# Kernel tuning notes

Measured on AMD Instinct MI355X. Metric: run time of the kernel, lower is better.

## Reference

```python
import jax, jax.numpy as jnp
import numpy as np

B, S, D, H, HD = 2, 1024, 1024, 16, 64
CKV, CQ, R, DFF, L, V = 256, 384, 32, 2816, 4, 32000
EPS = 1.1920929e-07  # torch RMSNorm default eps = finfo(float32).eps


def rmsnorm(x, w):
    return x * jax.lax.rsqrt(jnp.mean(x * x, -1, keepdims=True) + EPS) * w


def rope(x, base=10000.0):
    # x: [B, H, S, d]; GPT-NeoX style rotate-half, matches RoPE._neg_half
    d, s = x.shape[-1], x.shape[2]
    theta = 1.0 / base ** (jnp.arange(0, d, 2, dtype=jnp.float32) / d)
    ang = jnp.arange(s, dtype=jnp.float32)[:, None] * theta[None, :]
    ang = jnp.concatenate([ang, ang], -1)  # [s, d]
    neg = jnp.concatenate([-x[..., d // 2:], x[..., :d // 2]], -1)
    return x * jnp.cos(ang) + neg * jnp.sin(ang)


def forward(tokens, embed, w_kv_down, b_kv_down, w_q_down, b_q_down, w_kv_up, b_kv_up,
            w_q_up, b_q_up, w_o, b_o, kv_norm_w, q_norm_w, norm1_w, norm2_w,
            w_in, b_in, w_out, b_out, norm_f_w, w_head, b_head):
    h = embed[tokens]                                  # [B, S, D]
    causal = jnp.triu(jnp.ones((S, S), bool), 1)       # True above diagonal -> masked
    scale = np.float32(1.0 / np.sqrt(HD + R))
    for i in range(L):
        xn = rmsnorm(h, norm1_w[i])
        ckv = xn @ w_kv_down[i] + b_kv_down[i]         # [B, S, CKV+R]
        c_kv, k_rope = ckv[..., :CKV], ckv[..., CKV:]
        kv = rmsnorm(c_kv, kv_norm_w[i]) @ w_kv_up[i] + b_kv_up[i]
        kv = kv.reshape(B, S, H, 2 * HD).transpose(0, 2, 1, 3)  # [B, H, S, 2*HD]
        k, v = kv[..., :HD], kv[..., HD:]
        qf = rmsnorm(xn @ w_q_down[i] + b_q_down[i], q_norm_w[i]) @ w_q_up[i] + b_q_up[i]
        qf = qf.reshape(B, S, H, HD + R).transpose(0, 2, 1, 3)   # [B, H, S, HD+R]
        q, q_rope = qf[..., :HD], qf[..., HD:]
        k_rope = rope(k_rope[:, None, :, :])           # [B, 1, S, R], shared across heads
        q_rope = rope(q_rope)
        k = jnp.concatenate([k, jnp.broadcast_to(k_rope, (B, H, S, R))], -1)
        q = jnp.concatenate([q, q_rope], -1)
        a = jnp.einsum('bhqd,bhkd->bhqk', q, k) * scale
        a = jax.nn.softmax(jnp.where(causal, -jnp.inf, a), -1)
        attn = jnp.einsum('bhqk,bhkd->bhqd', a, v).transpose(0, 2, 1, 3).reshape(B, S, D)
        h = h + attn @ w_o[i] + b_o[i]
        uv = rmsnorm(h, norm2_w[i]) @ w_in[i] + b_in[i]  # [B, S, 2*DFF]
        h = h + (uv[..., :DFF] * jax.nn.silu(uv[..., DFF:])) @ w_out[i] + b_out[i]
    return rmsnorm(h, norm_f_w) @ w_head + b_head        # [B, S, V]


def setup_inputs() -> dict:
    key = jax.random.key(0)
    it = iter(jax.random.split(key, 24))
    w = lambda shp: jax.random.normal(next(it), shp, jnp.float32) * 0.02
    return dict(
        tokens=jax.random.randint(next(it), (B, S), 0, V),
        embed=w((V, D)),
        w_kv_down=w((L, D, CKV + R)), b_kv_down=w((L, CKV + R)),
        w_q_down=w((L, D, CQ)), b_q_down=w((L, CQ)),
        w_kv_up=w((L, CKV, 2 * HD * H)), b_kv_up=w((L, 2 * HD * H)),
        w_q_up=w((L, CQ, (HD + R) * H)), b_q_up=w((L, (HD + R) * H)),
        w_o=w((L, D, D)), b_o=w((L, D)),
        kv_norm_w=jnp.ones((L, CKV)), q_norm_w=jnp.ones((L, CQ)),
        norm1_w=jnp.ones((L, D)), norm2_w=jnp.ones((L, D)),
        w_in=w((L, D, 2 * DFF)), b_in=w((L, 2 * DFF)),
        w_out=w((L, DFF, D)), b_out=w((L, D)),
        norm_f_w=jnp.ones((D,)),
        w_head=w((D, V)), b_head=w((V,)),
    )


def reference(tokens, embed, w_kv_down, b_kv_down, w_q_down, b_q_down, w_kv_up, b_kv_up,
              w_q_up, b_q_up, w_o, b_o, kv_norm_w, q_norm_w, norm1_w, norm2_w,
              w_in, b_in, w_out, b_out, norm_f_w, w_head, b_head):
    return forward(tokens, embed, w_kv_down, b_kv_down, w_q_down, b_q_down, w_kv_up,
                   b_kv_up, w_q_up, b_q_up, w_o, b_o, kv_norm_w, q_norm_w, norm1_w,
                   norm2_w, w_in, b_in, w_out, b_out, norm_f_w, w_head, b_head)
```

## Files before the change

### kernel.cpp

```cpp
#include <hip/hip_runtime.h>
#include <cstdint>
#include <cstddef>

typedef unsigned short u16;
typedef __attribute__((__ext_vector_type__(8))) __bf16 bf16x8;
typedef __attribute__((__ext_vector_type__(4))) float f32x4;
typedef __attribute__((__ext_vector_type__(8))) unsigned short u16x8;

#define DEVI __device__ __forceinline__

constexpr int Bb = 2, Ss = 1024, Dd = 1024, Hh = 16;
constexpr int Mm = Bb * Ss;
constexpr int QKD = 128;
constexpr float EPSF = 1.1920929e-07f;
constexpr float NEG = -1e30f;
constexpr float QSCALE = 0.10206207261596577f;
constexpr float LOG1E4_16 = 9.210340371976184f / 16.f;

DEVI u16 f2b(float f) {
  union { float f; uint32_t u; } a; a.f = f;
  uint32_t r = a.u + 0x7FFFu + ((a.u >> 16) & 1u);
  return (u16)(r >> 16);
}
DEVI float b2f(u16 h) {
  union { uint32_t u; float f; } a; a.u = ((uint32_t)h) << 16; return a.f;
}

struct WJob { const float* src; u16* dst; int K; int N; int perm; int ntiles; };
struct WJobs { WJob j[7]; };

__global__ __launch_bounds__(256) void k_wcvt_batch(WJobs jobs, int njobs) {
  int t = blockIdx.x;
  int ji = 0;
  while (ji < njobs - 1 && t >= jobs.j[ji].ntiles) { t -= jobs.j[ji].ntiles; ++ji; }
  const float* __restrict__ src = jobs.j[ji].src;
  u16* __restrict__ dst = jobs.j[ji].dst;
  const int K = jobs.j[ji].K, N = jobs.j[ji].N, perm = jobs.j[ji].perm;
  const int ktiles = K >> 6;
  const int bk = (t % ktiles) * 64;
  const int bn = (t / ktiles) * 64;
  __shared__ float ts[64][65];
  const int tid = threadIdx.x;
  {
    int c4 = tid & 15, r = tid >> 4;
    #pragma unroll
    for (int p = 0; p < 4; ++p) {
      int row = r + p * 16;
      int col = bn + c4 * 4;
      float4 v = make_float4(0.f, 0.f, 0.f, 0.f);
      if (col < N) v = *(const float4*)(src + (size_t)(bk + row) * N + col);
      ts[row][c4 * 4 + 0] = v.x; ts[row][c4 * 4 + 1] = v.y;
      ts[row][c4 * 4 + 2] = v.z; ts[row][c4 * 4 + 3] = v.w;
    }
  }
  __syncthreads();
  {
    int k8 = tid & 7, c = tid >> 3;
    #pragma unroll
    for (int p = 0; p < 2; ++p) {
      int cc = c + p * 32;
      int gcol = bn + cc;
      int row = perm ? ((gcol < 2816) ? (gcol * 2) : ((gcol - 2816) * 2 + 1)) : gcol;
      u16x8 o;
      #pragma unroll
      for (int q = 0; q < 8; ++q) o[q] = f2b(ts[k8 * 8 + q][cc]);
      *(u16x8*)(dst + (size_t)row * K + bk + k8 * 8) = o;
    }
  }
}

__global__ void k_embed(const int* __restrict__ tok, const float* __restrict__ emb,
                        float* __restrict__ h) {
  int m = blockIdx.x;
  int t = tok[m];
  const float4* src = (const float4*)(emb + (size_t)t * Dd);
  float4* dst = (float4*)(h + (size_t)m * Dd);
  dst[threadIdx.x] = src[threadIdx.x];
}

__global__ void k_rms(const float* __restrict__ in, int inStride,
                      const float* __restrict__ w, u16* __restrict__ out, int K) {
  int m = blockIdx.x;
  const float* x = in + (size_t)m * inStride;
  float ss = 0.f;
  for (int i = threadIdx.x; i < K; i += 256) { float v = x[i]; ss += v * v; }
  #pragma unroll
  for (int off = 32; off; off >>= 1) ss += __shfl_xor(ss, off);
  __shared__ float red[4];
  if ((threadIdx.x & 63) == 0) red[threadIdx.x >> 6] = ss;
  __syncthreads();
  float r = rsqrtf((red[0] + red[1] + red[2] + red[3]) / (float)K + EPSF);
  for (int i = threadIdx.x; i < K; i += 256)
    out[(size_t)m * K + i] = f2b(x[i] * r * w[i]);
}

__global__ void k_rms2(const float* __restrict__ in, const float* __restrict__ w1,
                       const float* __restrict__ w2, u16* __restrict__ out1,
                       u16* __restrict__ out2) {
  int m = blockIdx.x;
  const float* x = in + (size_t)m * 768;
  int tid = threadIdx.x;
  __shared__ float red[4];
  {
    float v = x[tid];
    float ss = v * v;
    #pragma unroll
    for (int off = 32; off; off >>= 1) ss += __shfl_xor(ss, off);
    if ((tid & 63) == 0) red[tid >> 6] = ss;
    __syncthreads();
    float r = rsqrtf((red[0] + red[1] + red[2] + red[3]) / 256.f + EPSF);
    out1[(size_t)m * 256 + tid] = f2b(v * r * w1[tid]);
    __syncthreads();
  }
  {
    float v0 = x[384 + tid];
    float v1 = (tid < 128) ? x[640 + tid] : 0.f;
    float ss = v0 * v0 + v1 * v1;
    #pragma unroll
    for (int off = 32; off; off >>= 1) ss += __shfl_xor(ss, off);
    if ((tid & 63) == 0) red[tid >> 6] = ss;
    __syncthreads();
    float r = rsqrtf((red[0] + red[1] + red[2] + red[3]) / 384.f + EPSF);
    out2[(size_t)m * 384 + tid] = f2b(v0 * r * w2[tid]);
    if (tid < 128) out2[(size_t)m * 384 + 256 + tid] = f2b(v1 * r * w2[256 + tid]);
  }
}

__global__ void k_buildk(const u16* __restrict__ kv, const float* __restrict__ ckvq,
                         u16* __restrict__ Kb) {
  int s = blockIdx.x, bh = blockIdx.y;
  int b = bh >> 4, h = bh & 15;
  int d = threadIdx.x;
  int m = b * Ss + s;
  int j = d - 64;
  u16 kvv = 0;
  if (d < 64) kvv = kv[(size_t)m * 2048 + h * 128 + d];
  else if (d < 96) {
    float theta = __expf(-(float)(j & 15) * LOG1E4_16);
    float sn, cs;
    __sincosf((float)s * theta, &sn, &cs);
    const float* rr = ckvq + (size_t)m * 768 + 256;
    float x = rr[j], o = rr[j ^ 16];
    kvv = f2b(x * cs + ((j < 16) ? -o : o) * sn);
  }
  Kb[((size_t)bh * Ss + s) * QKD + d] = kvv;
}

__global__ void k_buildvt(const u16* __restrict__ kv, u16* __restrict__ Vt) {
  __shared__ u16 t[32][33];
  int bh = blockIdx.x, s0 = blockIdx.y * 32, d0 = blockIdx.z * 32;
  int b = bh >> 4, h = bh & 15;
  int tx = threadIdx.x, ty = threadIdx.y;
  #pragma unroll
  for (int i = ty; i < 32; i += 8) {
    int s = s0 + i, d = d0 + tx;
    t[i][tx] = kv[(size_t)(b * Ss + s) * 2048 + h * 128 + 64 + d];
  }
  __syncthreads();
  #pragma unroll
  for (int i = ty; i < 32; i += 8) {
    int d = d0 + i, s = s0 + tx;
    Vt[((size_t)bh * 64 + d) * Ss + s] = t[tx][i];
  }
}

#define GAS __attribute__((address_space(1)))
#define LAS __attribute__((address_space(3)))
DEVI void gll16(const void* g, void* l) {
  __builtin_amdgcn_global_load_lds((GAS const void*)g, (LAS void*)l, 16, 0, 0);
}
#define VMW(n) asm volatile("s_waitcnt vmcnt(" #n ")" ::: "memory")
#define FENCE asm volatile("" ::: "memory")

__global__ __launch_bounds__(256) void k_flash(
    const u16* __restrict__ qf, const u16* __restrict__ Kg,
    const u16* __restrict__ Vtg, u16* __restrict__ attn) {
  __shared__ u16 lK[2][64 * 128];
  __shared__ u16 lV[2][64 * 64];
  __shared__ u16 lP[4][16 * 64];
  const int tid = threadIdx.x;
  const int pair = blockIdx.x, bh = blockIdx.y;
  const int b = bh >> 4, h = bh & 15;
  const int lane = tid & 63, w = tid >> 6;
  const int g = lane >> 4, fr = lane & 15;
  const u16* Kh = Kg + (size_t)bh * Ss * QKD;
  const u16* Vh = Vtg + (size_t)bh * 64 * Ss;

  auto stageKV = [&](int buf, int kt) {
    int r = tid >> 4, c = tid & 15;
    #pragma unroll
    for (int gg = 0; gg < 4; ++gg) {
      int row = gg * 16 + r;
      const u16* src = Kh + (size_t)(kt * 64 + row) * QKD + ((c ^ (row & 7)) * 8);
      gll16(src, (u16*)lK[buf] + gg * 2048 + tid * 8);
    }
    int r2 = tid >> 3, c2 = tid & 7;
    #pragma unroll
    for (int gg = 0; gg < 2; ++gg) {
      int d = gg * 32 + r2;
      const u16* src = Vh + (size_t)d * Ss + kt * 64 + ((c2 ^ (d & 7)) * 8);
      gll16(src, (u16*)lV[buf] + gg * 2048 + tid * 8);
    }
  };

  for (int pass = 0; pass < 2; ++pass) {
    const int qt = pass ? (15 - pair) : pair;
    const int q0 = qt * 64;
    const int s_row = q0 + w * 16 + fr;
    const u16* qrow = qf + (size_t)(b * Ss + s_row) * 1536 + h * 96;
    bf16x8 af[4];
    {
      u16x8 r0 = *(const u16x8*)(qrow + g * 8);
      u16x8 r1 = *(const u16x8*)(qrow + 32 + g * 8);
      u16x8 r2 = *(const u16x8*)(qrow + 64 + g * 8);
      u16x8 a0, a1, a2, a3;
      #pragma unroll
      for (int q = 0; q < 8; ++q) {
        a0[q] = f2b(b2f(r0[q]) * QSCALE);
        a1[q] = f2b(b2f(r1[q]) * QSCALE);
        float x = b2f(r2[q]);
        float oth = __shfl_xor(x, 32);
        int jj = (g & 1) * 8 + q;
        float theta = __expf(-(float)jj * LOG1E4_16);
        float sn, cs;
        __sincosf((float)s_row * theta, &sn, &cs);
        float v = x * cs + ((g < 2) ? -oth : oth) * sn;
        a2[q] = f2b(v * QSCALE);
        a3[q] = 0;
      }
      af[0] = *(bf16x8*)&a0; af[1] = *(bf16x8*)&a1;
      af[2] = *(bf16x8*)&a2; af[3] = *(bf16x8*)&a3;
    }

    f32x4 acc_o[4] = {};
    float mrow = NEG, lrow = 0.f;

    stageKV(0, 0);

    for (int kt = 0; kt <= qt; ++kt) {
      const int cur = kt & 1;
      if (kt < qt) { stageKV(cur ^ 1, kt + 1); VMW(6); }
      else { VMW(0); }
      __builtin_amdgcn_s_barrier();
      FENCE;

      f32x4 accs[4] = {};
      #pragma unroll
      for (int j = 0; j < 4; ++j) {
        #pragma unroll
        for (int k4 = 0; k4 < 4; ++k4) {
          int row = j * 16 + fr;
          int ch = (k4 * 4 + g) ^ (row & 7);
          bf16x8 kf = *(const bf16x8*)&lK[cur][row * 128 + ch * 8];
          accs[j] = __builtin_amdgcn_mfma_f32_16x16x32_bf16(kf, af[k4], accs[j], 0, 0, 0);
        }
      }

      float p[16];
      float tmax = NEG;
      #pragma unroll
      for (int j = 0; j < 4; ++j)
        #pragma unroll
        for (int r = 0; r < 4; ++r) {
          float s = accs[j][r];
          int kloc = j * 16 + 4 * g + r;
          bool valid = (kt < qt) || (kloc <= w * 16 + fr);
          s = valid ? s : NEG;
          p[j * 4 + r] = s;
          tmax = fmaxf(tmax, s);
        }
      tmax = fmaxf(tmax, __shfl_xor(tmax, 16));
      tmax = fmaxf(tmax, __shfl_xor(tmax, 32));
      float mnew = fmaxf(mrow, tmax);
      float scale = __expf(mrow - mnew);
      float tsum = 0.f;
      #pragma unroll
      for (int i = 0; i < 16; ++i) { p[i] = __expf(p[i] - mnew); tsum += p[i]; }
      tsum += __shfl_xor(tsum, 16);
      tsum += __shfl_xor(tsum, 32);
      lrow = lrow * scale + tsum;
      mrow = mnew;

      #pragma unroll
      for (int j = 0; j < 4; ++j)
        #pragma unroll
        for (int t = 0; t < 2; ++t) {
          uint32_t u = (uint32_t)f2b(p[j * 4 + 2 * t]) |
                       ((uint32_t)f2b(p[j * 4 + 2 * t + 1]) << 16);
          int kp = 8 * j + 2 * g + t;
          int ch = kp >> 2, wi = kp & 3;
          ((uint32_t*)lP[w])[fr * 32 + ((ch ^ (fr & 7)) << 2) + wi] = u;
        }

      float sc_q[4];
      #pragma unroll
      for (int r = 0; r < 4; ++r) sc_q[r] = __shfl(scale, 4 * g + r);
      #pragma unroll
      for (int j2 = 0; j2 < 4; ++j2)
        #pragma unroll
        for (int r = 0; r < 4; ++r) acc_o[j2][r] *= sc_q[r];

      #pragma unroll
      for (int ksub = 0; ksub < 2; ++ksub) {
        int chp = (4 * ksub + g) ^ (fr & 7);
        bf16x8 pa = *(const bf16x8*)&((const u16*)lP[w])[fr * 64 + chp * 8];
        #pragma unroll
        for (int j2 = 0; j2 < 4; ++j2) {
          int d = j2 * 16 + fr;
          int chv = (ksub * 4 + g) ^ (d & 7);
          bf16x8 vf = *(const bf16x8*)&lV[cur][d * 64 + chv * 8];
          acc_o[j2] = __builtin_amdgcn_mfma_f32_16x16x32_bf16(pa, vf, acc_o[j2], 0, 0, 0);
        }
      }
      FENCE;
      __builtin_amdgcn_s_barrier();
      FENCE;
    }

    float li[4];
    #pragma unroll
    for (int r = 0; r < 4; ++r) li[r] = 1.f / __shfl(lrow, 4 * g + r);
    #pragma unroll
    for (int j2 = 0; j2 < 4; ++j2)
      #pragma unroll
      for (int r = 0; r < 4; ++r) {
        int q = q0 + w * 16 + 4 * g + r;
        int d = j2 * 16 + fr;
        attn[((size_t)(b * Ss) + q) * Dd + h * 64 + d] = f2b(acc_o[j2][r] * li[r]);
      }
  }
}

template <int MODE, int BM, int BN, int MINW = 4>
__global__ __launch_bounds__(256, MINW) void k_gemm(
    const u16* __restrict__ A, const u16* __restrict__ Bt,
    const float* __restrict__ bias, const float* __restrict__ bias2,
    void* __restrict__ C, int N, int K) {
  constexpr int MI = BM / 32, NJ = BN / 32;
  constexpr int AL = BM / 64, BL = BN / 64;
  __shared__ u16 lA[2][BM * 32];
  __shared__ u16 lB[2][BN * 32];
  const int tid = threadIdx.x;
  const int gx = gridDim.x;
  const int nwg = gx * gridDim.y;
  const int f = blockIdx.y * gx + blockIdx.x;
  const int f2 = (f & 7) * (nwg >> 3) + (f >> 3);
  const int bx = f2 % gx, by = f2 / gx;
  const long m0 = (long)bx * BM, n0 = (long)by * BN;
  const int lane = tid & 63, wid = tid >> 6;
  const int wm = (wid >> 1) * (BM / 2), wn = (wid & 1) * (BN / 2);
  const int fr = lane & 15, l4 = lane >> 4;
  const int sw = (fr >> 1) & 3;

  const int rs = tid >> 2;
  const int cs = ((tid & 3) ^ ((rs >> 1) & 3)) * 8;
  const u16* a0 = A + (m0 + rs) * (long)K + cs;
  const u16* b0 = Bt + (n0 + rs) * (long)K + cs;
  const long g64 = 64L * K;

  f32x4 acc[MI][NJ] = {};
  const int NT = K >> 5;

  auto stage = [&](int buf, int kk) {
    #pragma unroll
    for (int g = 0; g < AL; ++g)
      gll16(a0 + g * g64 + kk, (u16*)lA[buf] + g * 2048 + tid * 8);
    #pragma unroll
    for (int g = 0; g < BL; ++g)
      gll16(b0 + g * g64 + kk, (u16*)lB[buf] + g * 2048 + tid * 8);
  };

  stage(0, 0);

  for (int j = 0; j < NT; ++j) {
    const int cur = j & 1;
    const int kk1 = (j + 1) << 5;
    if (j + 1 < NT) {
      stage(cur ^ 1, kk1);
      if constexpr (AL + BL == 2) VMW(2);
      else if constexpr (AL + BL == 3) VMW(3);
      else if constexpr (AL + BL == 4) VMW(4);
      else if constexpr (AL + BL == 5) VMW(5);
      else VMW(6);
    } else {
      VMW(0);
    }
    __builtin_amdgcn_s_barrier();
    FENCE;
    bf16x8 af[MI], bfr[NJ];
    #pragma unroll
    for (int i = 0; i < MI; i++)
      af[i] = *(const bf16x8*)&lA[cur][(wm + i * 16 + fr) * 32 + ((l4 ^ sw) * 8)];
    #pragma unroll
    for (int jj = 0; jj < NJ; jj++)
      bfr[jj] = *(const bf16x8*)&lB[cur][(wn + jj * 16 + fr) * 32 + ((l4 ^ sw) * 8)];
    #pragma unroll
    for (int i = 0; i < MI; i++)
      #pragma unroll
      for (int jj = 0; jj < NJ; jj++)
        acc[i][jj] = __builtin_amdgcn_mfma_f32_16x16x32_bf16(af[i], bfr[jj], acc[i][jj], 0, 0, 0);
    FENCE;
    __builtin_amdgcn_s_barrier();
    FENCE;
  }

  const long r0 = m0 + wm + l4 * 4;
  const long c0 = n0 + wn + fr;
  if (MODE == 3) {
    u16* G = (u16*)C;
    #pragma unroll
    for (int j = 0; j < NJ; ++j) {
      long col = c0 + j * 16;
      int pcol = (int)((col & 1) ? (col >> 1) + 2816 : (col >> 1));
      float bs = bias[pcol];
      #pragma unroll
      for (int i = 0; i < MI; ++i)
        #pragma unroll
        for (int r = 0; r < 4; ++r) {
          float val = acc[i][j][r] + bs;
          float oth = __shfl_xor(val, 1);
          if (!(col & 1)) {
            float x = oth;
            float gv = val * x * (1.f / (1.f + __expf(-x)));
            G[(r0 + i * 16 + r) * 2816L + (col >> 1)] = f2b(gv);
          }
        }
    }
  } else {
    #pragma unroll
    for (int j = 0; j < NJ; ++j) {
      long col = c0 + j * 16;
      float bs;
      if (MODE == 4)
        bs = (col < 288) ? bias[col] : ((col >= 384) ? bias2[col - 384] : 0.f);
      else
        bs = bias[col];
      #pragma unroll
      for (int i = 0; i < MI; ++i)
        #pragma unroll
        for (int r = 0; r < 4; ++r) {
          long row = r0 + i * 16 + r;
          float val = acc[i][j][r] + bs;
          if (MODE == 0 || MODE == 4) ((float*)C)[row * N + col] = val;
          else if (MODE == 1) { float* p = (float*)C + row * N + col; *p += val; }
          else ((u16*)C)[row * N + col] = f2b(val);
        }
    }
  }
}

extern "C" void kernel_launch(void* const* d_in, const int* in_sizes, int n_in,
                              void* d_out, int out_size, void* d_ws, size_t ws_size,
                              hipStream_t stream) {
  (void)in_sizes; (void)n_in; (void)out_size; (void)ws_size;
  const int*   tokens    = (const int*)  d_in[0];
  const float* embed     = (const float*)d_in[1];
  const float* w_kv_down = (const float*)d_in[2];
  const float* b_kv_down = (const float*)d_in[3];
  const float* w_q_down  = (const float*)d_in[4];
  const float* b_q_down  = (const float*)d_in[5];
  const float* w_kv_up   = (const float*)d_in[6];
  const float* b_kv_up   = (const float*)d_in[7];
  const float* w_q_up    = (const float*)d_in[8];
  const float* b_q_up    = (const float*)d_in[9];
  const float* w_o       = (const float*)d_in[10];
  const float* b_o       = (const float*)d_in[11];
  const float* kv_norm_w = (const float*)d_in[12];
  const float* q_norm_w  = (const float*)d_in[13];
  const float* norm1_w   = (const float*)d_in[14];
  const float* norm2_w   = (const float*)d_in[15];
  const float* w_in      = (const float*)d_in[16];
  const float* b_in      = (const float*)d_in[17];
  const float* w_out     = (const float*)d_in[18];
  const float* b_out     = (const float*)d_in[19];
  const float* norm_f_w  = (const float*)d_in[20];
  const float* w_head    = (const float*)d_in[21];
  const float* b_head    = (const float*)d_in[22];

  char* base = (char*)d_ws;
  size_t off = 0;
  auto alloc = [&](size_t bytes) -> void* {
    void* p = base + off;
    off += (bytes + 255) & ~(size_t)255;
    return p;
  };
  u16* warena = (u16*)alloc((size_t)32000 * 1024 * 2);
  u16* wT_dq    = warena;
  u16* wT_kvup  = wT_dq   + 768 * 1024;
  u16* wT_qup   = wT_kvup + 2048 * 256;
  u16* wT_o     = wT_qup  + 1536 * 384;
  u16* wT_in    = wT_o    + 1024 * 1024;
  u16* wT_out   = wT_in   + 5632 * 1024;

  float* h     = (float*)alloc((size_t)Mm * 1024 * 4);
  u16*   xn    = (u16*)  alloc((size_t)Mm * 1024 * 2);
  float* ckvq  = (float*)alloc((size_t)Mm * 768 * 4);
  u16*   ckvn  = (u16*)  alloc((size_t)Mm * 256 * 2);
  u16*   kv    = (u16*)  alloc((size_t)Mm * 2048 * 2);
  u16*   qdn   = (u16*)  alloc((size_t)Mm * 384 * 2);
  u16*   qf    = (u16*)  alloc((size_t)Mm * 1536 * 2);
  u16*   Kb    = (u16*)  alloc((size_t)32 * 1024 * QKD * 2);
  u16*   Vt    = (u16*)  alloc((size_t)32 * 64 * 1024 * 2);
  u16*   attn  = (u16*)  alloc((size_t)Mm * 1024 * 2);
  u16*   gate  = (u16*)  alloc((size_t)Mm * 2816 * 2);

  dim3 tb(32, 8);

  k_embed<<<Mm, 256, 0, stream>>>(tokens, embed, h);

  for (int l = 0; l < 4; l++) {
    WJobs jb;
    jb.j[0] = { w_kv_down + (size_t)l * 1024 * 288,  wT_dq,              1024, 288,  0, 96 };
    jb.j[1] = { w_q_down  + (size_t)l * 1024 * 384,  wT_dq + 384 * 1024, 1024, 384,  0, 96 };
    jb.j[2] = { w_kv_up   + (size_t)l * 256 * 2048,  wT_kvup,            256,  2048, 0, 128 };
    jb.j[3] = { w_q_up    + (size_t)l * 384 * 1536,  wT_qup,             384,  1536, 0, 144 };
    jb.j[4] = { w_o       + (size_t)l * 1024 * 1024, wT_o,               1024, 1024, 0, 256 };
    jb.j[5] = { w_in      + (size_t)l * 1024 * 5632, wT_in,              1024, 5632, 1, 1408 };
    jb.j[6] = { w_out     + (size_t)l * 2816 * 1024, wT_out,             2816, 1024, 0, 704 };
    k_wcvt_batch<<<2832, 256, 0, stream>>>(jb, 7);

    k_rms<<<Mm, 256, 0, stream>>>(h, 1024, norm1_w + l * 1024, xn, 1024);
    k_gemm<4, 64, 64><<<dim3(32, 12), 256, 0, stream>>>(xn, wT_dq, b_kv_down + l * 288,
                                                        b_q_down + l * 384, ckvq, 768, 1024);
    k_rms2<<<Mm, 256, 0, stream>>>(ckvq, kv_norm_w + l * 256, q_norm_w + l * 384,
                                   ckvn, qdn);
    k_gemm<2, 64, 128><<<dim3(32, 16), 256, 0, stream>>>(ckvn, wT_kvup, b_kv_up + l * 2048,
                                                         nullptr, kv, 2048, 256);
    k_gemm<2, 64, 64><<<dim3(32, 24), 256, 0, stream>>>(qdn, wT_qup, b_q_up + l * 1536,
                                                        nullptr, qf, 1536, 384);
    k_buildk<<<dim3(Ss, 32), 128, 0, stream>>>(kv, ckvq, Kb);
    k_buildvt<<<dim3(32, 32, 2), tb, 0, stream>>>(kv, Vt);
    k_flash<<<dim3(8, 32), 256, 0, stream>>>(qf, Kb, Vt, attn);
    k_gemm<1, 64, 64><<<dim3(32, 16), 256, 0, stream>>>(attn, wT_o, b_o + l * 1024,
                                                        nullptr, h, 1024, 1024);
    k_rms<<<Mm, 256, 0, stream>>>(h, 1024, norm2_w + l * 1024, xn, 1024);
    k_gemm<3, 128, 128><<<dim3(16, 44), 256, 0, stream>>>(xn, wT_in, b_in + l * 5632,
                                                          nullptr, gate, 5632, 1024);
    k_gemm<1, 64, 64><<<dim3(32, 16), 256, 0, stream>>>(gate, wT_out, b_out + l * 1024,
                                                        nullptr, h, 1024, 2816);
  }

  k_rms<<<Mm, 256, 0, stream>>>(h, 1024, norm_f_w, xn, 1024);
  {
    WJobs jbh;
    jbh.j[0] = { w_head, warena, 1024, 32000, 0, 8000 };
    k_wcvt_batch<<<8000, 256, 0, stream>>>(jbh, 1);
  }
  k_gemm<0, 128, 128><<<dim3(16, 250), 256, 0, stream>>>(xn, warena, b_head,
                                                         nullptr, (float*)d_out, 32000, 1024);
}
```

Measured before the change: 1.027 ms.

## Batch weight conversion across layers and merge small kernels into paired launches

All four layers' weights are converted to bf16 in one launch up front instead of one launch per layer, using a per-layer slot in a larger arena. The kv-up and q-up GEMMs are merged into one launch that selects its job by grid z, and the K-build and V-transpose kernels are merged into one kernel. The aim is fewer launches and better GPU fill for the small kernels. The cost is a larger scratch arena and some idle blocks in the paired GEMM, since the q-up grid is smaller than the kv-up grid.

```diff
diff --git a/kernel.cpp b/kernel.cpp
--- a/kernel.cpp
+++ b/kernel.cpp
@@ -26,15 +26,18 @@
   union { uint32_t u; float f; } a; a.u = ((uint32_t)h) << 16; return a.f;
 }
 
-struct WJob { const float* src; u16* dst; int K; int N; int perm; int ntiles; };
+struct WJob { const float* src; u16* dst; long src_lstride; int K; int N; int perm; int ntiles; };
 struct WJobs { WJob j[7]; };
 
-__global__ __launch_bounds__(256) void k_wcvt_batch(WJobs jobs, int njobs) {
-  int t = blockIdx.x;
+__global__ __launch_bounds__(256) void k_wcvt_batch(WJobs jobs, int njobs,
+                                                    int tiles_per_layer, long dst_lstride) {
+  int bt = blockIdx.x;
+  int layer = bt / tiles_per_layer;
+  int t = bt - layer * tiles_per_layer;
   int ji = 0;
   while (ji < njobs - 1 && t >= jobs.j[ji].ntiles) { t -= jobs.j[ji].ntiles; ++ji; }
-  const float* __restrict__ src = jobs.j[ji].src;
-  u16* __restrict__ dst = jobs.j[ji].dst;
+  const float* __restrict__ src = jobs.j[ji].src + (size_t)layer * jobs.j[ji].src_lstride;
+  u16* __restrict__ dst = jobs.j[ji].dst + (size_t)layer * dst_lstride;
   const int K = jobs.j[ji].K, N = jobs.j[ji].N, perm = jobs.j[ji].perm;
   const int ktiles = K >> 6;
   const int bk = (t % ktiles) * 64;
@@ -126,41 +129,41 @@
   }
 }
 
-__global__ void k_buildk(const u16* __restrict__ kv, const float* __restrict__ ckvq,
-                         u16* __restrict__ Kb) {
-  int s = blockIdx.x, bh = blockIdx.y;
+__global__ void k_buildkv(const u16* __restrict__ kv, const float* __restrict__ ckvq,
+                          u16* __restrict__ Kb, u16* __restrict__ Vt) {
+  int bh = blockIdx.x, chunk = blockIdx.y, role = blockIdx.z;
   int b = bh >> 4, h = bh & 15;
-  int d = threadIdx.x;
-  int m = b * Ss + s;
-  int j = d - 64;
-  u16 kvv = 0;
-  if (d < 64) kvv = kv[(size_t)m * 2048 + h * 128 + d];
-  else if (d < 96) {
-    float theta = __expf(-(float)(j & 15) * LOG1E4_16);
-    float sn, cs;
-    __sincosf((float)s * theta, &sn, &cs);
-    const float* rr = ckvq + (size_t)m * 768 + 256;
-    float x = rr[j], o = rr[j ^ 16];
-    kvv = f2b(x * cs + ((j < 16) ? -o : o) * sn);
-  }
-  Kb[((size_t)bh * Ss + s) * QKD + d] = kvv;
-}
-
-__global__ void k_buildvt(const u16* __restrict__ kv, u16* __restrict__ Vt) {
-  __shared__ u16 t[32][33];
-  int bh = blockIdx.x, s0 = blockIdx.y * 32, d0 = blockIdx.z * 32;
-  int b = bh >> 4, h = bh & 15;
-  int tx = threadIdx.x, ty = threadIdx.y;
-  #pragma unroll
-  for (int i = ty; i < 32; i += 8) {
-    int s = s0 + i, d = d0 + tx;
-    t[i][tx] = kv[(size_t)(b * Ss + s) * 2048 + h * 128 + 64 + d];
-  }
-  __syncthreads();
-  #pragma unroll
-  for (int i = ty; i < 32; i += 8) {
-    int d = d0 + i, s = s0 + tx;
-    Vt[((size_t)bh * 64 + d) * Ss + s] = t[tx][i];
+  if (role < 2) {
+    __shared__ u16 t[32][33];
+    int tx = threadIdx.x & 31, ty = threadIdx.x >> 5;
+    int s0 = chunk * 32, d0 = role * 32;
+    #pragma unroll
+    for (int i = ty; i < 32; i += 8)
+      t[i][tx] = kv[(size_t)(b * Ss + s0 + i) * 2048 + h * 128 + 64 + d0 + tx];
+    __syncthreads();
+    #pragma unroll
+    for (int i = ty; i < 32; i += 8)
+      Vt[((size_t)bh * 64 + d0 + i) * Ss + s0 + tx] = t[tx][i];
+  } else {
+    int idx = threadIdx.x;
+    int d = idx & 127, r0 = idx >> 7;
+    #pragma unroll
+    for (int it = 0; it < 16; ++it) {
+      int s = chunk * 32 + it * 2 + r0;
+      int m = b * Ss + s;
+      u16 kvv = 0;
+      if (d < 64) kvv = kv[(size_t)m * 2048 + h * 128 + d];
+      else if (d < 96) {
+        int j = d - 64;
+        float theta = __expf(-(float)(j & 15) * LOG1E4_16);
+        float sn, cs;
+        __sincosf((float)s * theta, &sn, &cs);
+        const float* rr = ckvq + (size_t)m * 768 + 256;
+        float x = rr[j], o = rr[j ^ 16];
+        kvv = f2b(x * cs + ((j < 16) ? -o : o) * sn);
+      }
+      Kb[((size_t)bh * Ss + s) * QKD + d] = kvv;
+    }
   }
 }
 
@@ -331,21 +334,15 @@
   }
 }
 
-template <int MODE, int BM, int BN, int MINW = 4>
-__global__ __launch_bounds__(256, MINW) void k_gemm(
-    const u16* __restrict__ A, const u16* __restrict__ Bt,
-    const float* __restrict__ bias, const float* __restrict__ bias2,
-    void* __restrict__ C, int N, int K) {
+template <int MODE, int BM, int BN>
+DEVI void gemm_core(const u16* __restrict__ A, const u16* __restrict__ Bt,
+                    const float* __restrict__ bias, const float* __restrict__ bias2,
+                    void* __restrict__ C, int N, int K, int bx, int by,
+                    u16* lA, u16* lB) {
   constexpr int MI = BM / 32, NJ = BN / 32;
   constexpr int AL = BM / 64, BL = BN / 64;
-  __shared__ u16 lA[2][BM * 32];
-  __shared__ u16 lB[2][BN * 32];
+  constexpr int ASZ = BM * 32, BSZ = BN * 32;
   const int tid = threadIdx.x;
-  const int gx = gridDim.x;
-  const int nwg = gx * gridDim.y;
-  const int f = blockIdx.y * gx + blockIdx.x;
-  const int f2 = (f & 7) * (nwg >> 3) + (f >> 3);
-  const int bx = f2 % gx, by = f2 / gx;
   const long m0 = (long)bx * BM, n0 = (long)by * BN;
   const int lane = tid & 63, wid = tid >> 6;
   const int wm = (wid >> 1) * (BM / 2), wn = (wid & 1) * (BN / 2);
@@ -364,10 +361,10 @@
   auto stage = [&](int buf, int kk) {
     #pragma unroll
     for (int g = 0; g < AL; ++g)
-      gll16(a0 + g * g64 + kk, (u16*)lA[buf] + g * 2048 + tid * 8);
+      gll16(a0 + g * g64 + kk, lA + buf * ASZ + g * 2048 + tid * 8);
     #pragma unroll
     for (int g = 0; g < BL; ++g)
-      gll16(b0 + g * g64 + kk, (u16*)lB[buf] + g * 2048 + tid * 8);
+      gll16(b0 + g * g64 + kk, lB + buf * BSZ + g * 2048 + tid * 8);
   };
 
   stage(0, 0);
@@ -390,10 +387,10 @@
     bf16x8 af[MI], bfr[NJ];
     #pragma unroll
     for (int i = 0; i < MI; i++)
-      af[i] = *(const bf16x8*)&lA[cur][(wm + i * 16 + fr) * 32 + ((l4 ^ sw) * 8)];
+      af[i] = *(const bf16x8*)&lA[cur * ASZ + (wm + i * 16 + fr) * 32 + ((l4 ^ sw) * 8)];
     #pragma unroll
     for (int jj = 0; jj < NJ; jj++)
-      bfr[jj] = *(const bf16x8*)&lB[cur][(wn + jj * 16 + fr) * 32 + ((l4 ^ sw) * 8)];
+      bfr[jj] = *(const bf16x8*)&lB[cur * BSZ + (wn + jj * 16 + fr) * 32 + ((l4 ^ sw) * 8)];
     #pragma unroll
     for (int i = 0; i < MI; i++)
       #pragma unroll
@@ -447,6 +444,38 @@
         }
     }
   }
+}
+
+template <int MODE, int BM, int BN, int MINW = 4>
+__global__ __launch_bounds__(256, MINW) void k_gemm(
+    const u16* __restrict__ A, const u16* __restrict__ Bt,
+    const float* __restrict__ bias, const float* __restrict__ bias2,
+    void* __restrict__ C, int N, int K) {
+  __shared__ u16 lA[2 * BM * 32];
+  __shared__ u16 lB[2 * BN * 32];
+  const int gx = gridDim.x;
+  const int nwg = gx * gridDim.y;
+  const int f = blockIdx.y * gx + blockIdx.x;
+  const int f2 = (f & 7) * (nwg >> 3) + (f >> 3);
+  const int bx = f2 % gx, by = f2 / gx;
+  gemm_core<MODE, BM, BN>(A, Bt, bias, bias2, C, N, K, bx, by, lA, lB);
+}
+
+__global__ __launch_bounds__(256, 4) void k_gemm_pair(
+    const u16* A0, const u16* Bt0, const float* b0, void* C0, int N0, int K0, int gy0,
+    const u16* A1, const u16* Bt1, const float* b1, void* C1, int N1, int K1, int gy1) {
+  __shared__ u16 lA[2 * 64 * 32];
+  __shared__ u16 lB[2 * 128 * 32];
+  const int z = blockIdx.z;
+  const int gy = z ? gy1 : gy0;
+  if ((int)blockIdx.y >= gy) return;
+  const int gx = gridDim.x;
+  const int nwg = gx * gy;
+  const int f = blockIdx.y * gx + blockIdx.x;
+  const int f2 = (f & 7) * (nwg >> 3) + (f >> 3);
+  const int bx = f2 % gx, by = f2 / gx;
+  if (z) gemm_core<2, 64, 128>(A1, Bt1, b1, nullptr, C1, N1, K1, bx, by, lA, lB);
+  else   gemm_core<2, 64, 128>(A0, Bt0, b0, nullptr, C0, N0, K0, bx, by, lA, lB);
 }
 
 extern "C" void kernel_launch(void* const* d_in, const int* in_sizes, int n_in,
@@ -484,13 +513,9 @@
     off += (bytes + 255) & ~(size_t)255;
     return p;
   };
-  u16* warena = (u16*)alloc((size_t)32000 * 1024 * 2);
-  u16* wT_dq    = warena;
-  u16* wT_kvup  = wT_dq   + 768 * 1024;
-  u16* wT_qup   = wT_kvup + 2048 * 256;
-  u16* wT_o     = wT_qup  + 1536 * 384;
-  u16* wT_in    = wT_o    + 1024 * 1024;
-  u16* wT_out   = wT_in   + 5632 * 1024;
+  const long O_DQ = 0, O_KVUP = 786432, O_QUP = 1310720, O_O = 1900544,
+             O_IN = 2949120, O_OUT = 8716288, LSLOT = 11599872;
+  u16* warena = (u16*)alloc((size_t)4 * LSLOT * 2);
 
   float* h     = (float*)alloc((size_t)Mm * 1024 * 4);
   u16*   xn    = (u16*)  alloc((size_t)Mm * 1024 * 2);
@@ -504,32 +529,38 @@
   u16*   attn  = (u16*)  alloc((size_t)Mm * 1024 * 2);
   u16*   gate  = (u16*)  alloc((size_t)Mm * 2816 * 2);
 
-  dim3 tb(32, 8);
-
   k_embed<<<Mm, 256, 0, stream>>>(tokens, embed, h);
 
+  {
+    WJobs jb;
+    jb.j[0] = { w_kv_down, warena + O_DQ,              1024L * 288,  1024, 288,  0, 96 };
+    jb.j[1] = { w_q_down,  warena + O_DQ + 384 * 1024, 1024L * 384,  1024, 384,  0, 96 };
+    jb.j[2] = { w_kv_up,   warena + O_KVUP,            256L * 2048,  256,  2048, 0, 128 };
+    jb.j[3] = { w_q_up,    warena + O_QUP,             384L * 1536,  384,  1536, 0, 144 };
+    jb.j[4] = { w_o,       warena + O_O,               1024L * 1024, 1024, 1024, 0, 256 };
+    jb.j[5] = { w_in,      warena + O_IN,              1024L * 5632, 1024, 5632, 1, 1408 };
+    jb.j[6] = { w_out,     warena + O_OUT,             2816L * 1024, 2816, 1024, 0, 704 };
+    k_wcvt_batch<<<4 * 2832, 256, 0, stream>>>(jb, 7, 2832, LSLOT);
+  }
+
   for (int l = 0; l < 4; l++) {
-    WJobs jb;
-    jb.j[0] = { w_kv_down + (size_t)l * 1024 * 288,  wT_dq,              1024, 288,  0, 96 };
-    jb.j[1] = { w_q_down  + (size_t)l * 1024 * 384,  wT_dq + 384 * 1024, 1024, 384,  0, 96 };
-    jb.j[2] = { w_kv_up   + (size_t)l * 256 * 2048,  wT_kvup,            256,  2048, 0, 128 };
-    jb.j[3] = { w_q_up    + (size_t)l * 384 * 1536,  wT_qup,             384,  1536, 0, 144 };
-    jb.j[4] = { w_o       + (size_t)l * 1024 * 1024, wT_o,               1024, 1024, 0, 256 };
-    jb.j[5] = { w_in      + (size_t)l * 1024 * 5632, wT_in,              1024, 5632, 1, 1408 };
-    jb.j[6] = { w_out     + (size_t)l * 2816 * 1024, wT_out,             2816, 1024, 0, 704 };
-    k_wcvt_batch<<<2832, 256, 0, stream>>>(jb, 7);
+    u16* wl = warena + (size_t)l * LSLOT;
+    u16* wT_dq  = wl + O_DQ;
+    u16* wT_kvup = wl + O_KVUP;
+    u16* wT_qup = wl + O_QUP;
+    u16* wT_o   = wl + O_O;
+    u16* wT_in  = wl + O_IN;
+    u16* wT_out = wl + O_OUT;
 
     k_rms<<<Mm, 256, 0, stream>>>(h, 1024, norm1_w + l * 1024, xn, 1024);
     k_gemm<4, 64, 64><<<dim3(32, 12), 256, 0, stream>>>(xn, wT_dq, b_kv_down + l * 288,
                                                         b_q_down + l * 384, ckvq, 768, 1024);
     k_rms2<<<Mm, 256, 0, stream>>>(ckvq, kv_norm_w + l * 256, q_norm_w + l * 384,
                                    ckvn, qdn);
-    k_gemm<2, 64, 128><<<dim3(32, 16), 256, 0, stream>>>(ckvn, wT_kvup, b_kv_up + l * 2048,
-                                                         nullptr, kv, 2048, 256);
-    k_gemm<2, 64, 64><<<dim3(32, 24), 256, 0, stream>>>(qdn, wT_qup, b_q_up + l * 1536,
-                                                        nullptr, qf, 1536, 384);
-    k_buildk<<<dim3(Ss, 32), 128, 0, stream>>>(kv, ckvq, Kb);
-    k_buildvt<<<dim3(32, 32, 2), tb, 0, stream>>>(kv, Vt);
+    k_gemm_pair<<<dim3(32, 16, 2), 256, 0, stream>>>(
+        ckvn, wT_kvup, b_kv_up + l * 2048, kv, 2048, 256, 16,
+        qdn,  wT_qup,  b_q_up + l * 1536,  qf, 1536, 384, 12);
+    k_buildkv<<<dim3(32, 32, 3), 256, 0, stream>>>(kv, ckvq, Kb, Vt);
     k_flash<<<dim3(8, 32), 256, 0, stream>>>(qf, Kb, Vt, attn);
     k_gemm<1, 64, 64><<<dim3(32, 16), 256, 0, stream>>>(attn, wT_o, b_o + l * 1024,
                                                         nullptr, h, 1024, 1024);
@@ -543,8 +574,8 @@
   k_rms<<<Mm, 256, 0, stream>>>(h, 1024, norm_f_w, xn, 1024);
   {
     WJobs jbh;
-    jbh.j[0] = { w_head, warena, 1024, 32000, 0, 8000 };
-    k_wcvt_batch<<<8000, 256, 0, stream>>>(jbh, 1);
+    jbh.j[0] = { w_head, warena, 0, 1024, 32000, 0, 8000 };
+    k_wcvt_batch<<<8000, 256, 0, stream>>>(jbh, 1, 8000, 0);
   }
   k_gemm<0, 128, 128><<<dim3(16, 250), 256, 0, stream>>>(xn, warena, b_head,
                                                          nullptr, (float*)d_out, 32000, 1024);
```

Result: faster. 986.0 us (median of 2 runs) (-4.0%).
